# Kernel optimization log

Hardware: AMD Instinct MI355X
Metric: run time of the kernel (lower is better)

## Reference

```python
import jax, jax.numpy as jnp
import numpy as np

HIDDEN = 1024
NUM_SLOTS = 8
VOCAB = 32768
B, T = 32, 2048


def setup_inputs() -> dict:
    key = jax.random.key(0)
    k1, k2, k3 = jax.random.split(key, 3)
    hidden_states = jax.random.normal(k1, (B, T, HIDDEN), dtype=jnp.float32)
    attention_mask = jnp.ones((B, T), dtype=jnp.int32)
    # slot projector weight, torch Linear stores [out, in] = [H*num_slots, H]
    W_proj = jax.random.normal(k2, (HIDDEN * NUM_SLOTS, HIDDEN), dtype=jnp.float32) * 0.02
    codebook = jax.random.normal(k3, (VOCAB, HIDDEN), dtype=jnp.float32) * 0.02
    return {"hidden_states": hidden_states, "attention_mask": attention_mask,
            "W_proj": W_proj, "codebook": codebook}


def _masked_mean(states, mask):
    # states [B,T,H], mask [B,T] -> [B,H]
    w = mask.astype(states.dtype)
    denom = jnp.clip(w.sum(axis=1, keepdims=True), 1.0)
    return jnp.einsum('bth,bt->bh', states, w) / denom


def reference(hidden_states, attention_mask, W_proj, codebook):
    pooled = _masked_mean(hidden_states, attention_mask)          # [B,H]
    pre_q = (pooled @ W_proj.T).reshape(-1, NUM_SLOTS, HIDDEN)    # [B,S,H]
    distances = (jnp.sum(pre_q ** 2, axis=-1, keepdims=True)
                 - 2.0 * jnp.einsum('bsh,vh->bsv', pre_q, codebook)
                 + jnp.sum(codebook ** 2, axis=-1)[None, None, :])  # [B,S,V]
    logits = -distances
    indices = jnp.argmax(logits, axis=-1)                         # [B,S]
    embedded = codebook[indices]                                  # [B,S,H]
    quantized = pre_q + jax.lax.stop_gradient(embedded - pre_q)
    commitment_loss = jnp.mean((pre_q - jax.lax.stop_gradient(embedded)) ** 2)
    codebook_loss = jnp.mean((embedded - jax.lax.stop_gradient(pre_q)) ** 2)
    return logits, indices, pre_q, quantized, commitment_loss, codebook_loss
```

## Files before the change

kernel.cpp:

```cpp
#include <hip/hip_runtime.h>
#include <hip/hip_bf16.h>

#define B_ 32
#define T_ 2048
#define H_ 1024
#define S_ 8
#define V_ 32768
#define ROWS 256
#define OUTO 8192
#define NCHUNK 64
#define TCHUNK 32
#define NCB 256
#define DELTA2 0.008f
#define MAXCAND 512

typedef __attribute__((ext_vector_type(8))) short s16x8;
typedef __attribute__((ext_vector_type(8))) unsigned short u16x8;
typedef __attribute__((ext_vector_type(4))) float f32x4;

__device__ __forceinline__ void gl_lds16(const void* gsrc, void* ldst) {
  __builtin_amdgcn_global_load_lds(
      (const __attribute__((address_space(1))) unsigned int*)gsrc,
      (__attribute__((address_space(3))) unsigned int*)ldst, 16, 0, 0);
}

__device__ __forceinline__ unsigned short bf16hi(float x) {
  return __builtin_bit_cast(unsigned short, __float2bfloat16(x));
}

__global__ void pool_kernel(const float* __restrict__ hidden,
                            const int* __restrict__ mask,
                            float* __restrict__ part_pool,
                            int* __restrict__ cntpart) {
  int b = blockIdx.x;
  int chunk = blockIdx.y;
  int t0 = chunk * TCHUNK;
  int h4 = threadIdx.x * 4;
  const float* base = hidden + ((size_t)b * T_ + t0) * H_ + h4;
  const int* mrow = mask + (size_t)b * T_ + t0;
  float a0 = 0.f, a1 = 0.f, a2 = 0.f, a3 = 0.f;
  int mcount = 0;
#pragma unroll 4
  for (int i = 0; i < TCHUNK; ++i) {
    int mi = mrow[i];
    float m = (float)mi;
    mcount += mi;
    float4 v = *reinterpret_cast<const float4*>(base + (size_t)i * H_);
    a0 += m * v.x; a1 += m * v.y; a2 += m * v.z; a3 += m * v.w;
  }
  float* pp = part_pool + ((size_t)chunk * B_ + b) * H_ + h4;
  *reinterpret_cast<float4*>(pp) = make_float4(a0, a1, a2, a3);
  if (threadIdx.x == 0) cntpart[chunk * B_ + b] = mcount;
}

__global__ void pool_reduce_kernel(const float* __restrict__ part_pool,
                                   const int* __restrict__ cntpart,
                                   float* __restrict__ pooledT,
                                   int* __restrict__ cnt) {
  int g = blockIdx.x * 256 + threadIdx.x;
  float s = 0.f;
  for (int c = 0; c < NCHUNK; ++c) s += part_pool[(size_t)c * (H_ * B_) + g];
  int b = g >> 10, h = g & 1023;
  pooledT[h * B_ + b] = s;
  if (g < B_) {
    int cs = 0;
    for (int c = 0; c < NCHUNK; ++c) cs += cntpart[c * B_ + g];
    cnt[g] = cs;
  }
}

__global__ __launch_bounds__(256) void proj_kernel(const float* __restrict__ Wp,
                            const float* __restrict__ pooledT,
                            const int* __restrict__ cnt,
                            float* __restrict__ preq) {
  __shared__ float pl[32][516];
  const int t = threadIdx.x;
  const int og = t >> 5, b = t & 31;
  const int o0 = blockIdx.x * 32;
  float acc0 = 0.f, acc1 = 0.f, acc2 = 0.f, acc3 = 0.f;
  const float* wb = Wp + (size_t)(o0 + og * 4) * H_;
  for (int pass = 0; pass < 2; ++pass) {
    int k0 = pass * 512;
    __syncthreads();
#pragma unroll
    for (int i = 0; i < 16; ++i) {
      int f = i * 1024 + t * 4;
      int hl = f >> 5, b4 = f & 31;
      float4 v = *reinterpret_cast<const float4*>(&pooledT[(size_t)(k0 + hl) * 32 + b4]);
      pl[b4 + 0][hl] = v.x; pl[b4 + 1][hl] = v.y;
      pl[b4 + 2][hl] = v.z; pl[b4 + 3][hl] = v.w;
    }
    __syncthreads();
    const float* w0 = wb + k0;
#pragma unroll 4
    for (int j = 0; j < 128; ++j) {
      float4 p = *reinterpret_cast<const float4*>(&pl[b][4 * j]);
      float4 a = *reinterpret_cast<const float4*>(w0 + 4 * j);
      float4 c = *reinterpret_cast<const float4*>(w0 + H_ + 4 * j);
      float4 d = *reinterpret_cast<const float4*>(w0 + 2 * H_ + 4 * j);
      float4 e = *reinterpret_cast<const float4*>(w0 + 3 * H_ + 4 * j);
      acc0 += a.x * p.x + a.y * p.y + a.z * p.z + a.w * p.w;
      acc1 += c.x * p.x + c.y * p.y + c.z * p.z + c.w * p.w;
      acc2 += d.x * p.x + d.y * p.y + d.z * p.z + d.w * p.w;
      acc3 += e.x * p.x + e.y * p.y + e.z * p.z + e.w * p.w;
    }
  }
  float denom = fmaxf((float)cnt[b], 1.0f);
  size_t obase = (size_t)b * OUTO + o0 + og * 4;
  preq[obase + 0] = acc0 / denom;
  preq[obase + 1] = acc1 / denom;
  preq[obase + 2] = acc2 / denom;
  preq[obase + 3] = acc3 / denom;
}

__global__ void aprep_kernel(const float* __restrict__ preq,
                             unsigned short* __restrict__ A_img,
                             float* __restrict__ xnorm) {
  int row = blockIdx.x;
  int t = threadIdx.x;
  int k0 = 4 * t;
  int ks = k0 >> 5, kk = k0 & 31;
  float4 v = reinterpret_cast<const float4*>(preq + (size_t)row * H_)[t];
  float xv[4] = {v.x, v.y, v.z, v.w};
  unsigned short hv[4];
  float s = 0.f;
#pragma unroll
  for (int i = 0; i < 4; ++i) { s += xv[i] * xv[i]; hv[i] = bf16hi(xv[i]); }
  unsigned int sidx = (unsigned int)(row * 32 + kk) ^ (unsigned int)((row & 7) << 3);
  *reinterpret_cast<ushort4*>(&A_img[(size_t)ks * 8192 + sidx]) =
      make_ushort4(hv[0], hv[1], hv[2], hv[3]);
#pragma unroll
  for (int off = 1; off < 64; off <<= 1) s += __shfl_xor(s, off);
  __shared__ float ps[4];
  if ((t & 63) == 0) ps[t >> 6] = s;
  __syncthreads();
  if (t == 0) xnorm[row] = ps[0] + ps[1] + ps[2] + ps[3];
}

__global__ __launch_bounds__(512, 2) void dist_kernel(
    const unsigned short* __restrict__ A_img, const float* __restrict__ codebook,
    const float* __restrict__ xnorm, float* __restrict__ logits,
    float* __restrict__ pscore) {
  __shared__ __align__(16) unsigned short Asm[2][8192];
  __shared__ __align__(16) unsigned short Bs[2][128][40];
  __shared__ float cn[128];
  __shared__ float xns[256];
  __shared__ float bwv[2][256];

  const int t = threadIdx.x;
  const int l = t & 63;
  const int w = t >> 6;
  const int cb = w & 1;
  const int m0 = (w >> 1) * 64;
  const int lr = l & 15, lq = l >> 4;
  const int blk = blockIdx.x;
  const int v0 = blk * 128;

  if (t < 256) xns[t] = xnorm[t];

  const int sn = t >> 2;
  const int sk = (t & 3) * 8;
  const float* cbp = codebook + (size_t)(v0 + sn) * H_ + sk;
  float csq = 0.f;

  f32x4 acc[4][4];
#pragma unroll
  for (int i = 0; i < 4; ++i)
#pragma unroll
    for (int j = 0; j < 4; ++j) acc[i][j] = (f32x4){0.f, 0.f, 0.f, 0.f};

  const char* Abase = (const char*)A_img;

  unsigned int aoff[4];
#pragma unroll
  for (int mt = 0; mt < 4; ++mt) {
    int row = m0 + mt * 16 + lr;
    aoff[mt] = (unsigned int)(row * 32 + lq * 8) ^ (unsigned int)((row & 7) << 3);
  }

#define CONVERT_TO(BUF, X0, X1)                                                   \
  {                                                                               \
    float xv[8] = {X0.x, X0.y, X0.z, X0.w, X1.x, X1.y, X1.z, X1.w};               \
    u16x8 hv;                                                                     \
    _Pragma("unroll")                                                             \
    for (int i = 0; i < 8; ++i) { float x = xv[i]; csq += x * x; hv[i] = bf16hi(x); } \
    *reinterpret_cast<u16x8*>(&Bs[BUF][sn][sk]) = hv;                             \
  }

#define STAGE_A(KS, BUF)                                                          \
  _Pragma("unroll")                                                               \
  for (int j = 0; j < 2; ++j) {                                                   \
    int c = w * 2 + j;                                                            \
    gl_lds16(Abase + (size_t)(KS) * 16384 + (size_t)c * 1024 + (size_t)l * 16,    \
             &Asm[BUF][c * 512]);                                                 \
  }

#define DIST_STEP(KS, RT0, RT1, RS0, RS1)                                         \
  {                                                                               \
    const int curb = (KS) & 1, nxt = curb ^ 1;                                    \
    if ((KS) < 31) STAGE_A((KS) + 1, nxt);                                        \
    if ((KS) < 30) {                                                              \
      RT0 = *reinterpret_cast<const float4*>(cbp + ((KS) + 2) * 32);              \
      RT1 = *reinterpret_cast<const float4*>(cbp + ((KS) + 2) * 32 + 4);          \
    }                                                                             \
    s16x8 ah[4], bh[4];                                                           \
    _Pragma("unroll")                                                             \
    for (int nt = 0; nt < 4; ++nt)                                                \
      bh[nt] = *reinterpret_cast<const s16x8*>(&Bs[curb][cb * 64 + nt * 16 + lr][lq * 8]); \
    _Pragma("unroll")                                                             \
    for (int mt = 0; mt < 4; ++mt)                                                \
      ah[mt] = *reinterpret_cast<const s16x8*>(&Asm[curb][aoff[mt]]);             \
    __builtin_amdgcn_s_setprio(1);                                                \
    _Pragma("unroll")                                                             \
    for (int mt = 0; mt < 4; ++mt)                                                \
      _Pragma("unroll")                                                           \
      for (int nt = 0; nt < 4; ++nt)                                              \
        acc[mt][nt] = __builtin_amdgcn_mfma_f32_16x16x32_bf16(ah[mt], bh[nt], acc[mt][nt], 0, 0, 0); \
    __builtin_amdgcn_s_setprio(0);                                                \
    if ((KS) < 31) CONVERT_TO(nxt, RS0, RS1);                                     \
    __syncthreads();                                                              \
  }

  STAGE_A(0, 0);
  float4 ra0 = *reinterpret_cast<const float4*>(cbp);
  float4 ra1 = *reinterpret_cast<const float4*>(cbp + 4);
  float4 rb0 = *reinterpret_cast<const float4*>(cbp + 32);
  float4 rb1 = *reinterpret_cast<const float4*>(cbp + 36);
  CONVERT_TO(0, ra0, ra1);
  __syncthreads();

#pragma unroll 1
  for (int ks = 0; ks < 32; ks += 2) {
    DIST_STEP(ks,     ra0, ra1, rb0, rb1);
    DIST_STEP(ks + 1, rb0, rb1, ra0, ra1);
  }

  csq += __shfl_xor(csq, 1);
  csq += __shfl_xor(csq, 2);
  if ((t & 3) == 0) cn[sn] = csq;
  __syncthreads();

  const float NEG = -3.402823466e38f;
#pragma unroll
  for (int mt = 0; mt < 4; ++mt) {
#pragma unroll
    for (int r = 0; r < 4; ++r) {
      int row = m0 + mt * 16 + lq * 4 + r;
      float xn = xns[row];
      float bs = NEG;
#pragma unroll
      for (int nt = 0; nt < 4; ++nt) {
        int col = cb * 64 + nt * 16 + lr;
        float sc = 2.f * acc[mt][nt][r] - cn[col];
        logits[(size_t)row * V_ + v0 + col] = sc - xn;
        bs = fmaxf(bs, sc);
      }
#pragma unroll
      for (int off = 1; off < 16; off <<= 1) bs = fmaxf(bs, __shfl_xor(bs, off));
      if (lr == 0) bwv[cb][row] = bs;
    }
  }
  __syncthreads();
  if (t < 256) pscore[(size_t)t * NCB + blk] = fmaxf(bwv[0][t], bwv[1][t]);
}

__global__ __launch_bounds__(256) void finalize_kernel(
    const float* __restrict__ preq, const float* __restrict__ codebook,
    const float* __restrict__ logits, const float* __restrict__ xnorm,
    const float* __restrict__ pscore,
    float* __restrict__ out_idx, float* __restrict__ out_quant,
    float* __restrict__ lsum) {
  int row = blockIdx.x;
  int t = threadIdx.x;
  float m = pscore[(size_t)row * NCB + t];
#pragma unroll
  for (int off = 1; off < 64; off <<= 1) m = fmaxf(m, __shfl_xor(m, off));
  __shared__ float wm[4];
  if ((t & 63) == 0) wm[t >> 6] = m;
  __syncthreads();
  float M = fmaxf(fmaxf(wm[0], wm[1]), fmaxf(wm[2], wm[3]));
  float thr = M - xnorm[row] - DELTA2;
  __shared__ int cand[MAXCAND];
  __shared__ int ncand;
  if (t == 0) ncand = 0;
  __syncthreads();
  const float* lrow = logits + (size_t)row * V_;
#pragma unroll 4
  for (int it = 0; it < 32; ++it) {
    int c0 = it * 1024 + t * 4;
    float4 lg = *reinterpret_cast<const float4*>(lrow + c0);
    if (lg.x >= thr) { int p = atomicAdd(&ncand, 1); if (p < MAXCAND) cand[p] = c0; }
    if (lg.y >= thr) { int p = atomicAdd(&ncand, 1); if (p < MAXCAND) cand[p] = c0 + 1; }
    if (lg.z >= thr) { int p = atomicAdd(&ncand, 1); if (p < MAXCAND) cand[p] = c0 + 2; }
    if (lg.w >= thr) { int p = atomicAdd(&ncand, 1); if (p < MAXCAND) cand[p] = c0 + 3; }
  }
  __syncthreads();
  int total = ncand;
  const float* pr = preq + (size_t)row * H_;
  int idx;
  if (total <= MAXCAND) {
    __shared__ double sd[4];
    double best = -1.0e300; int bi = V_;
    for (int j = 0; j < total; ++j) {
      int c = cand[j];
      const float* cr = codebook + (size_t)c * H_;
      float4 cv = reinterpret_cast<const float4*>(cr)[t];
      float4 pv = reinterpret_cast<const float4*>(pr)[t];
      double p = (double)cv.x * (2.0 * (double)pv.x - (double)cv.x)
               + (double)cv.y * (2.0 * (double)pv.y - (double)cv.y)
               + (double)cv.z * (2.0 * (double)pv.z - (double)cv.z)
               + (double)cv.w * (2.0 * (double)pv.w - (double)cv.w);
#pragma unroll
      for (int off = 1; off < 64; off <<= 1) p += __shfl_xor(p, off);
      if ((t & 63) == 0) sd[t >> 6] = p;
      __syncthreads();
      double s = sd[0] + sd[1] + sd[2] + sd[3];
      if (s > best || (s == best && c < bi)) { best = s; bi = c; }
      __syncthreads();
    }
    idx = bi;
  } else {
    double best = -1.0e300; int bi = V_;
    for (int c = t; c < V_; c += 256) {
      const float* cr = codebook + (size_t)c * H_;
      double s = 0.0;
      for (int k = 0; k < H_; k += 4) {
        float4 cv = *reinterpret_cast<const float4*>(cr + k);
        float4 pv = *reinterpret_cast<const float4*>(pr + k);
        s += (double)cv.x * (2.0 * (double)pv.x - (double)cv.x)
           + (double)cv.y * (2.0 * (double)pv.y - (double)cv.y)
           + (double)cv.z * (2.0 * (double)pv.z - (double)cv.z)
           + (double)cv.w * (2.0 * (double)pv.w - (double)cv.w);
      }
      if (s > best || (s == best && c < bi)) { best = s; bi = c; }
    }
#pragma unroll
    for (int off = 1; off < 64; off <<= 1) {
      double os = __shfl_xor(best, off);
      int oi = __shfl_xor(bi, off);
      if (os > best || (os == best && oi < bi)) { best = os; bi = oi; }
    }
    __shared__ double fb[4]; __shared__ int fbi[4];
    if ((t & 63) == 0) { fb[t >> 6] = best; fbi[t >> 6] = bi; }
    __syncthreads();
    double b0 = fb[0]; int i0 = fbi[0];
    for (int wv = 1; wv < 4; ++wv)
      if (fb[wv] > b0 || (fb[wv] == b0 && fbi[wv] < i0)) { b0 = fb[wv]; i0 = fbi[wv]; }
    idx = i0;
  }
  if (t == 0) out_idx[row] = (float)idx;
  float4 e = reinterpret_cast<const float4*>(codebook + (size_t)idx * H_)[t];
  float4 p4 = reinterpret_cast<const float4*>(pr)[t];
  float4 q;
  q.x = p4.x + (e.x - p4.x); q.y = p4.y + (e.y - p4.y);
  q.z = p4.z + (e.z - p4.z); q.w = p4.w + (e.w - p4.w);
  reinterpret_cast<float4*>(out_quant)[row * 256 + t] = q;
  float dx = p4.x - e.x, dy = p4.y - e.y, dz = p4.z - e.z, dw = p4.w - e.w;
  float ls = dx * dx + dy * dy + dz * dz + dw * dw;
#pragma unroll
  for (int off = 1; off < 64; off <<= 1) ls += __shfl_xor(ls, off);
  __shared__ float lss[4];
  if ((t & 63) == 0) lss[t >> 6] = ls;
  __syncthreads();
  if (t == 0) lsum[row] = lss[0] + lss[1] + lss[2] + lss[3];
}

__global__ void loss_kernel(const float* __restrict__ lsum, float* __restrict__ out_loss) {
  int t = threadIdx.x;
  float s = lsum[t];
#pragma unroll
  for (int off = 1; off < 64; off <<= 1) s += __shfl_xor(s, off);
  __shared__ float a[4];
  if ((t & 63) == 0) a[t >> 6] = s;
  __syncthreads();
  if (t == 0) {
    float lv = (a[0] + a[1] + a[2] + a[3]) / (float)(ROWS * H_);
    out_loss[0] = lv; out_loss[1] = lv;
  }
}

extern "C" void kernel_launch(void* const* d_in, const int* in_sizes, int n_in,
                              void* d_out, int out_size, void* d_ws, size_t ws_size,
                              hipStream_t stream) {
  (void)in_sizes; (void)n_in; (void)out_size; (void)ws_size;
  const float* hidden   = (const float*)d_in[0];
  const int* mask       = (const int*)d_in[1];
  const float* Wp       = (const float*)d_in[2];
  const float* codebook = (const float*)d_in[3];

  float* out = (float*)d_out;
  float* out_logits = out;
  float* out_idx    = out + 8388608;
  float* out_preq   = out_idx + 256;
  float* out_quant  = out_preq + 262144;
  float* out_loss   = out_quant + 262144;

  float* part_pool = out_logits;
  int*   cntpart   = (int*)(out_logits + 2097152);
  float* pooledT   = out_logits + 2099200;
  int*   cnt       = (int*)(out_logits + 2131968);

  float* ws     = (float*)d_ws;
  float* xnorm  = ws;
  float* pscore = ws + 256;
  float* lsum   = ws + 65792;
  unsigned short* A_img = (unsigned short*)(ws + 66048);

  pool_kernel<<<dim3(B_, NCHUNK), 256, 0, stream>>>(hidden, mask, part_pool, cntpart);
  pool_reduce_kernel<<<128, 256, 0, stream>>>(part_pool, cntpart, pooledT, cnt);
  proj_kernel<<<256, 256, 0, stream>>>(Wp, pooledT, cnt, out_preq);
  aprep_kernel<<<ROWS, 256, 0, stream>>>(out_preq, A_img, xnorm);
  dist_kernel<<<NCB, 512, 0, stream>>>(A_img, codebook, xnorm, out_logits, pscore);
  finalize_kernel<<<ROWS, 256, 0, stream>>>(out_preq, codebook, out_logits, xnorm,
                                            pscore, out_idx, out_quant, lsum);
  loss_kernel<<<1, 256, 0, stream>>>(lsum, out_loss);
}
```

Before: 196.4 us.

## Load A operand directly from global into registers, drop LDS staging

New measurement: 197.4 us. About the same (+0.5%).

```diff
diff --git a/kernel.cpp b/kernel.cpp
--- a/kernel.cpp
+++ b/kernel.cpp
@@ -17,12 +17,6 @@
 typedef __attribute__((ext_vector_type(8))) short s16x8;
 typedef __attribute__((ext_vector_type(8))) unsigned short u16x8;
 typedef __attribute__((ext_vector_type(4))) float f32x4;
-
-__device__ __forceinline__ void gl_lds16(const void* gsrc, void* ldst) {
-  __builtin_amdgcn_global_load_lds(
-      (const __attribute__((address_space(1))) unsigned int*)gsrc,
-      (__attribute__((address_space(3))) unsigned int*)ldst, 16, 0, 0);
-}
 
 __device__ __forceinline__ unsigned short bf16hi(float x) {
   return __builtin_bit_cast(unsigned short, __float2bfloat16(x));
@@ -126,8 +120,7 @@
   float s = 0.f;
 #pragma unroll
   for (int i = 0; i < 4; ++i) { s += xv[i] * xv[i]; hv[i] = bf16hi(xv[i]); }
-  unsigned int sidx = (unsigned int)(row * 32 + kk) ^ (unsigned int)((row & 7) << 3);
-  *reinterpret_cast<ushort4*>(&A_img[(size_t)ks * 8192 + sidx]) =
+  *reinterpret_cast<ushort4*>(&A_img[(size_t)ks * 8192 + row * 32 + kk]) =
       make_ushort4(hv[0], hv[1], hv[2], hv[3]);
 #pragma unroll
   for (int off = 1; off < 64; off <<= 1) s += __shfl_xor(s, off);
@@ -141,7 +134,6 @@
     const unsigned short* __restrict__ A_img, const float* __restrict__ codebook,
     const float* __restrict__ xnorm, float* __restrict__ logits,
     float* __restrict__ pscore) {
-  __shared__ __align__(16) unsigned short Asm[2][8192];
   __shared__ __align__(16) unsigned short Bs[2][128][40];
   __shared__ float cn[128];
   __shared__ float xns[256];
@@ -169,16 +161,17 @@
 #pragma unroll
     for (int j = 0; j < 4; ++j) acc[i][j] = (f32x4){0.f, 0.f, 0.f, 0.f};
 
-  const char* Abase = (const char*)A_img;
-
   unsigned int aoff[4];
 #pragma unroll
-  for (int mt = 0; mt < 4; ++mt) {
-    int row = m0 + mt * 16 + lr;
-    aoff[mt] = (unsigned int)(row * 32 + lq * 8) ^ (unsigned int)((row & 7) << 3);
-  }
-
-#define CONVERT_TO(BUF, X0, X1)                                                   \
+  for (int mt = 0; mt < 4; ++mt)
+    aoff[mt] = (unsigned int)((m0 + mt * 16 + lr) * 32 + lq * 8);
+
+#define LOAD_A(DST, KS)                                                           \
+  _Pragma("unroll")                                                               \
+  for (int mt = 0; mt < 4; ++mt)                                                  \
+    DST[mt] = *reinterpret_cast<const s16x8*>(&A_img[(size_t)(KS) * 8192 + aoff[mt]]);
+
+#define CONV(BUF, X0, X1)                                                         \
   {                                                                               \
     float xv[8] = {X0.x, X0.y, X0.z, X0.w, X1.x, X1.y, X1.z, X1.w};               \
     u16x8 hv;                                                                     \
@@ -187,52 +180,76 @@
     *reinterpret_cast<u16x8*>(&Bs[BUF][sn][sk]) = hv;                             \
   }
 
-#define STAGE_A(KS, BUF)                                                          \
-  _Pragma("unroll")                                                               \
-  for (int j = 0; j < 2; ++j) {                                                   \
-    int c = w * 2 + j;                                                            \
-    gl_lds16(Abase + (size_t)(KS) * 16384 + (size_t)c * 1024 + (size_t)l * 16,    \
-             &Asm[BUF][c * 512]);                                                 \
-  }
-
-#define DIST_STEP(KS, RT0, RT1, RS0, RS1)                                         \
+#define BAR()                                                                     \
+  asm volatile("s_waitcnt lgkmcnt(0)" ::: "memory");                              \
+  __builtin_amdgcn_s_barrier();                                                   \
+  __builtin_amdgcn_sched_barrier(0);
+
+#define STEP(KS, AU, AN, CC0, CC1, CL0, CL1)                                      \
   {                                                                               \
-    const int curb = (KS) & 1, nxt = curb ^ 1;                                    \
-    if ((KS) < 31) STAGE_A((KS) + 1, nxt);                                        \
-    if ((KS) < 30) {                                                              \
-      RT0 = *reinterpret_cast<const float4*>(cbp + ((KS) + 2) * 32);              \
-      RT1 = *reinterpret_cast<const float4*>(cbp + ((KS) + 2) * 32 + 4);          \
-    }                                                                             \
-    s16x8 ah[4], bh[4];                                                           \
+    LOAD_A(AN, (KS) + 1);                                                         \
+    int kl = (KS) + 3; if (kl > 31) kl = 31;                                      \
+    CL0 = *reinterpret_cast<const float4*>(cbp + kl * 32);                        \
+    CL1 = *reinterpret_cast<const float4*>(cbp + kl * 32 + 4);                    \
+    s16x8 bh[4];                                                                  \
     _Pragma("unroll")                                                             \
     for (int nt = 0; nt < 4; ++nt)                                                \
-      bh[nt] = *reinterpret_cast<const s16x8*>(&Bs[curb][cb * 64 + nt * 16 + lr][lq * 8]); \
-    _Pragma("unroll")                                                             \
-    for (int mt = 0; mt < 4; ++mt)                                                \
-      ah[mt] = *reinterpret_cast<const s16x8*>(&Asm[curb][aoff[mt]]);             \
+      bh[nt] = *reinterpret_cast<const s16x8*>(&Bs[(KS) & 1][cb * 64 + nt * 16 + lr][lq * 8]); \
     __builtin_amdgcn_s_setprio(1);                                                \
     _Pragma("unroll")                                                             \
     for (int mt = 0; mt < 4; ++mt)                                                \
       _Pragma("unroll")                                                           \
       for (int nt = 0; nt < 4; ++nt)                                              \
-        acc[mt][nt] = __builtin_amdgcn_mfma_f32_16x16x32_bf16(ah[mt], bh[nt], acc[mt][nt], 0, 0, 0); \
+        acc[mt][nt] = __builtin_amdgcn_mfma_f32_16x16x32_bf16(AU[mt], bh[nt], acc[mt][nt], 0, 0, 0); \
     __builtin_amdgcn_s_setprio(0);                                                \
-    if ((KS) < 31) CONVERT_TO(nxt, RS0, RS1);                                     \
-    __syncthreads();                                                              \
-  }
-
-  STAGE_A(0, 0);
-  float4 ra0 = *reinterpret_cast<const float4*>(cbp);
-  float4 ra1 = *reinterpret_cast<const float4*>(cbp + 4);
-  float4 rb0 = *reinterpret_cast<const float4*>(cbp + 32);
-  float4 rb1 = *reinterpret_cast<const float4*>(cbp + 36);
-  CONVERT_TO(0, ra0, ra1);
-  __syncthreads();
-
-#pragma unroll 1
-  for (int ks = 0; ks < 32; ks += 2) {
-    DIST_STEP(ks,     ra0, ra1, rb0, rb1);
-    DIST_STEP(ks + 1, rb0, rb1, ra0, ra1);
+    CONV(((KS) + 1) & 1, CC0, CC1);                                               \
+    BAR();                                                                        \
+  }
+
+  s16x8 a0[4], a1[4], a2[4];
+  LOAD_A(a0, 0);
+  float4 c00 = *reinterpret_cast<const float4*>(cbp);
+  float4 c01 = *reinterpret_cast<const float4*>(cbp + 4);
+  float4 c10 = *reinterpret_cast<const float4*>(cbp + 32);
+  float4 c11 = *reinterpret_cast<const float4*>(cbp + 36);
+  float4 c20 = *reinterpret_cast<const float4*>(cbp + 64);
+  float4 c21 = *reinterpret_cast<const float4*>(cbp + 68);
+  CONV(0, c00, c01);
+  BAR();
+
+  for (int ks = 0; ks < 30; ks += 3) {
+    STEP(ks,     a0, a1, c10, c11, c00, c01);
+    STEP(ks + 1, a1, a2, c20, c21, c10, c11);
+    STEP(ks + 2, a2, a0, c00, c01, c20, c21);
+  }
+  {
+    LOAD_A(a1, 31);
+    s16x8 bh[4];
+#pragma unroll
+    for (int nt = 0; nt < 4; ++nt)
+      bh[nt] = *reinterpret_cast<const s16x8*>(&Bs[0][cb * 64 + nt * 16 + lr][lq * 8]);
+    __builtin_amdgcn_s_setprio(1);
+#pragma unroll
+    for (int mt = 0; mt < 4; ++mt)
+#pragma unroll
+      for (int nt = 0; nt < 4; ++nt)
+        acc[mt][nt] = __builtin_amdgcn_mfma_f32_16x16x32_bf16(a0[mt], bh[nt], acc[mt][nt], 0, 0, 0);
+    __builtin_amdgcn_s_setprio(0);
+    CONV(1, c10, c11);
+    BAR();
+  }
+  {
+    s16x8 bh[4];
+#pragma unroll
+    for (int nt = 0; nt < 4; ++nt)
+      bh[nt] = *reinterpret_cast<const s16x8*>(&Bs[1][cb * 64 + nt * 16 + lr][lq * 8]);
+    __builtin_amdgcn_s_setprio(1);
+#pragma unroll
+    for (int mt = 0; mt < 4; ++mt)
+#pragma unroll
+      for (int nt = 0; nt < 4; ++nt)
+        acc[mt][nt] = __builtin_amdgcn_mfma_f32_16x16x32_bf16(a1[mt], bh[nt], acc[mt][nt], 0, 0, 0);
+    __builtin_amdgcn_s_setprio(0);
   }
 
   csq += __shfl_xor(csq, 1);
```
